# Kernel tuning notes

Hardware: AMD Instinct MI355X
Metric: run time of the kernel (lower is better)

The kernel has to match this reference:

```python
import jax, jax.numpy as jnp
import numpy as np

B, T, S = 256, 32, 128
I, H, O = 256, 1024, 256


def setup_inputs() -> dict:
    key = jax.random.key(0)
    ks = jax.random.split(key, 8)
    sc = 0.02
    return {
        "shifted_target": jax.random.normal(ks[0], (B, T, I), jnp.float32),
        "encoder_outputs": jax.random.normal(ks[1], (B, S, H), jnp.float32),
        "W_ih": jax.random.normal(ks[2], (4 * H, I), jnp.float32) * sc,
        "W_hh": jax.random.normal(ks[3], (4 * H, H), jnp.float32) * sc,
        "b_ih": jax.random.normal(ks[4], (4 * H,), jnp.float32) * sc,
        "b_hh": jax.random.normal(ks[5], (4 * H,), jnp.float32) * sc,
        "W_fc": jax.random.normal(ks[6], (O, 2 * H), jnp.float32) * sc,
        "b_fc": jax.random.normal(ks[7], (O,), jnp.float32) * sc,
    }


def reference(shifted_target, encoder_outputs, W_ih, W_hh, b_ih, b_hh, W_fc, b_fc):
    bs, tgt_len, inp = shifted_target.shape
    hid = encoder_outputs.shape[-1]
    # torch code feeds zeros (not shifted_target[:,0]) at t=0, with zero init state
    xs = shifted_target.at[:, 0, :].set(0.0)
    xs = jnp.swapaxes(xs, 0, 1)  # [T, B, I]

    def step(carry, x_t):
        h, c = carry
        gates = x_t @ W_ih.T + b_ih + h @ W_hh.T + b_hh  # [B, 4H]
        i, f, g, o = jnp.split(gates, 4, axis=-1)
        i = jax.nn.sigmoid(i)
        f = jax.nn.sigmoid(f)
        g = jnp.tanh(g)
        o = jax.nn.sigmoid(o)
        c = f * c + i * g
        h = o * jnp.tanh(c)
        # dot-product attention against encoder states
        score = jnp.einsum('bh,bsh->bs', h, encoder_outputs)
        prob = jax.nn.softmax(score, axis=-1)
        ctx = jnp.einsum('bs,bsh->bh', prob, encoder_outputs)
        out_t = jnp.concatenate([ctx, h], axis=-1) @ W_fc.T + b_fc
        return (h, c), (out_t, prob)

    h0 = jnp.zeros((bs, hid), shifted_target.dtype)
    c0 = jnp.zeros((bs, hid), shifted_target.dtype)
    _, (outs, probs) = jax.lax.scan(step, (h0, c0), xs)
    return jnp.swapaxes(outs, 0, 1), jnp.swapaxes(probs, 0, 1)
```

## Files before the change

### kernel.cpp

```cpp
#include <hip/hip_runtime.h>
#include <math.h>

#define B_  256
#define T_  32
#define S_  128
#define I_  256
#define H_  1024
#define O_  256
#define G4  4096
#define K2  2048

typedef __attribute__((ext_vector_type(8))) short bf16x8;
typedef __attribute__((ext_vector_type(4))) float f32x4;
typedef __attribute__((ext_vector_type(4))) unsigned u32x4;

#define MFMA16(a, b, c) __builtin_amdgcn_mfma_f32_16x16x32_bf16(a, b, c, 0, 0, 0)

__device__ __forceinline__ unsigned short f2bf(float f) {
    unsigned int u = __float_as_uint(f);
    u = (u + 0x7FFFu + ((u >> 16) & 1u)) >> 16;
    return (unsigned short)u;
}
__device__ __forceinline__ float sigm(float x) { return 1.0f / (1.0f + __expf(-x)); }

__device__ __forceinline__ void stg_sys128(unsigned short* p, u32x4 v) {
    asm volatile("global_store_dwordx4 %0, %1, off sc0 sc1"
                 :: "v"(p), "v"(v) : "memory");
}
__device__ __forceinline__ unsigned ldg_flag(const unsigned* p) {
    unsigned r;
    asm volatile("global_load_dword %0, %1, off sc0 sc1\n\ts_waitcnt vmcnt(0)"
                 : "=v"(r) : "v"(p) : "memory");
    return r;
}
__device__ __forceinline__ void stg_flag(unsigned* p, unsigned v) {
    asm volatile("global_store_dword %0, %1, off sc0 sc1"
                 :: "v"(p), "v"(v) : "memory");
}

__global__ void prep_kernel(
    const float* __restrict__ x, const float* __restrict__ enc,
    const float* __restrict__ Wih, const float* __restrict__ Whh,
    const float* __restrict__ bih, const float* __restrict__ bhh,
    const float* __restrict__ Wfc,
    unsigned short* __restrict__ WihR, unsigned short* __restrict__ WhhR,
    unsigned short* __restrict__ WfcR, float* __restrict__ biasR,
    unsigned short* __restrict__ xs, unsigned short* __restrict__ encB,
    unsigned short* __restrict__ h0,
    unsigned* __restrict__ bar)
{
    if (blockIdx.x == 0 && threadIdx.x < 256) bar[threadIdx.x] = 0u;

    const long NWHH = (long)G4 * H_;
    const long NWIH = (long)G4 * I_;
    const long NWFC = (long)O_ * K2;
    const long NB   = G4;
    const long NX   = (long)B_ * T_ * I_;
    const long NE   = (long)B_ * S_ * H_;
    const long NH   = (long)B_ * H_;
    const long total = NWHH + NWIH + NWFC + NB + NX + NE + NH;
    for (long i = (long)blockIdx.x * blockDim.x + threadIdx.x; i < total;
         i += (long)gridDim.x * blockDim.x) {
        long j = i;
        if (j < NE) { encB[j] = f2bf(enc[j]); continue; }
        j -= NE;
        if (j < NWHH) {
            int r = (int)(j >> 10), k = (int)(j & 1023);
            int n = ((r & 1023) << 2) | (r >> 10);
            WhhR[(long)n * H_ + k] = f2bf(Whh[j]);
            continue;
        }
        j -= NWHH;
        if (j < NWIH) {
            int r = (int)(j >> 8), k = (int)(j & 255);
            int n = ((r & 1023) << 2) | (r >> 10);
            WihR[(long)n * I_ + k] = f2bf(Wih[j]);
            continue;
        }
        j -= NWIH;
        if (j < NWFC) { WfcR[j] = f2bf(Wfc[j]); continue; }
        j -= NWFC;
        if (j < NB) {
            int r = (int)j;
            int n = ((r & 1023) << 2) | (r >> 10);
            biasR[n] = bih[r] + bhh[r];
            continue;
        }
        j -= NB;
        if (j < NX) {
            int t = (int)((j >> 8) & 31);
            xs[j] = (t == 0) ? (unsigned short)0 : f2bf(x[j]);
            continue;
        }
        j -= NX;
        h0[j] = 0;
    }
}

__global__ __launch_bounds__(512, 2) void steps_kernel(
    const unsigned short* __restrict__ xs,
    const unsigned short* __restrict__ WihR,
    const unsigned short* __restrict__ WhhR,
    const float* __restrict__ biasR,
    const unsigned short* __restrict__ h0b,
    unsigned short* __restrict__ hall,
    unsigned* __restrict__ bar)
{
    __shared__ unsigned short Wlds[64 * 1024];
    __shared__ float Gs[64 * 68];
    __shared__ unsigned short Hs[64 * 16];

    const int tid = threadIdx.x;
    const int lane = tid & 63, wave = tid >> 6;
    const int quad = lane >> 4, l16 = lane & 15;
    const int wm = wave >> 2, wn = wave & 3;

    const int id = blockIdx.x;
    const int xcd = id & 7, slot = id >> 3;
    const int nt = slot >> 2, mt = slot & 3;
    const int n0 = (xcd * 8 + nt) * 64;
    const int m0 = mt * 64;

    unsigned* myflag = bar + mt * 64 + xcd * 8 + nt;
    const unsigned* gflags = bar + mt * 64;

    for (int i = 0; i < 16; i++) {
        int q = i * 512 + tid;
        int row = q >> 7, kc = q & 127;
        int e = kc * 8;
        int de = row * 1024 + (e ^ ((row & 7) << 3));
        *(u32x4*)(Wlds + de) = *(const u32x4*)(WhhR + (long)(n0 + row) * H_ + e);
    }

    const int nw = n0 + wn * 16 + l16;
    bf16x8 bwx[8];
    {
        const unsigned short* px = WihR + (long)nw * I_ + quad * 8;
#pragma unroll
        for (int kk = 0; kk < 8; kk++) bwx[kk] = *(const bf16x8*)(px + kk * 32);
    }
    const float bj = biasR[nw];

    const unsigned short* bbase = Wlds + (wn * 16 + l16) * 1024;
    const int swz = (l16 & 7) << 3;

    int arow[2];
    const unsigned short* xrow[2];
#pragma unroll
    for (int i = 0; i < 2; i++) {
        arow[i] = m0 + wm * 32 + i * 16 + l16;
        xrow[i] = xs + (long)arow[i] * T_ * I_ + quad * 8;
    }

    float c_reg[2] = {0.f, 0.f};

    __syncthreads();

#pragma unroll 1
    for (int t = 0; t < T_; t++) {
        const f32x4 z = {0.f, 0.f, 0.f, 0.f};
        f32x4 acc[2] = {z, z};

        {
            bf16x8 a[8][2];
#pragma unroll
            for (int kk = 0; kk < 8; kk++)
#pragma unroll
                for (int i = 0; i < 2; i++)
                    a[kk][i] = *(const bf16x8*)(xrow[i] + (long)t * I_ + kk * 32);
#pragma unroll
            for (int kk = 0; kk < 8; kk++)
#pragma unroll
                for (int i = 0; i < 2; i++)
                    acc[i] = MFMA16(a[kk][i], bwx[kk], acc[i]);
        }

        if (t > 0) {
            if (tid < 64) {
                int spins = 0;
                while (ldg_flag(gflags + tid) < (unsigned)t &&
                       spins < (1 << 20)) {
                    __builtin_amdgcn_s_sleep(1);
                    ++spins;
                }
            }
            __syncthreads();
        }

        const unsigned short* hb;
        long hstr;
        if (t == 0) { hb = h0b;                      hstr = H_; }
        else        { hb = hall + (long)(t - 1) * H_; hstr = (long)T_ * H_; }
        const unsigned short* rp0 = hb + (long)arow[0] * hstr + quad * 8;
        const unsigned short* rp1 = hb + (long)arow[1] * hstr + quad * 8;

        {
            bf16x8 aa[2][4][2];
#pragma unroll
            for (int kk = 0; kk < 4; kk++) {
                aa[0][kk][0] = *(const bf16x8*)(rp0 + kk * 32);
                aa[0][kk][1] = *(const bf16x8*)(rp1 + kk * 32);
            }
#pragma unroll
            for (int sc = 0; sc < 8; sc++) {
                const int cur = sc & 1, nxt = cur ^ 1;
                if (sc < 7) {
                    const int kb = (sc + 1) * 4;
#pragma unroll
                    for (int kk = 0; kk < 4; kk++) {
                        aa[nxt][kk][0] = *(const bf16x8*)(rp0 + (kb + kk) * 32);
                        aa[nxt][kk][1] = *(const bf16x8*)(rp1 + (kb + kk) * 32);
                    }
                }
#pragma unroll
                for (int kk = 0; kk < 4; kk++) {
                    int e = ((sc * 4 + kk) * 32 + quad * 8) ^ swz;
                    bf16x8 bb = *(const bf16x8*)(bbase + e);
                    acc[0] = MFMA16(aa[cur][kk][0], bb, acc[0]);
                    acc[1] = MFMA16(aa[cur][kk][1], bb, acc[1]);
                }
            }
        }

#pragma unroll
        for (int i = 0; i < 2; i++)
#pragma unroll
            for (int r = 0; r < 4; r++)
                Gs[(wm * 32 + i * 16 + quad * 4 + r) * 68 + wn * 16 + l16] =
                    acc[i][r] + bj;
        __syncthreads();

#pragma unroll
        for (int j = 0; j < 2; j++) {
            int p = j * 512 + tid;
            int row = p >> 4, u = p & 15;
            float gi = Gs[row * 68 + u * 4 + 0];
            float gf = Gs[row * 68 + u * 4 + 1];
            float gg = Gs[row * 68 + u * 4 + 2];
            float go = Gs[row * 68 + u * 4 + 3];
            float ii = sigm(gi), ff = sigm(gf), g3 = tanhf(gg), oo = sigm(go);
            float cn = ff * c_reg[j] + ii * g3;
            float hh = oo * tanhf(cn);
            c_reg[j] = cn;
            Hs[row * 16 + u] = f2bf(hh);
        }
        __syncthreads();

        if (tid < 128) {
            int row = tid >> 1, half = tid & 1;
            u32x4 v = *(const u32x4*)(Hs + row * 16 + half * 8);
            unsigned short* dst = hall +
                ((long)(m0 + row) * T_ + t) * H_ + (n0 >> 2) + half * 8;
            stg_sys128(dst, v);
        }

        if (t < T_ - 1) {
            asm volatile("s_waitcnt vmcnt(0)" ::: "memory");
            __syncthreads();
            if (tid == 0) stg_flag(myflag, (unsigned)(t + 1));
        }
    }
}

__global__ __launch_bounds__(256) void scores_kernel(
    const unsigned short* __restrict__ hall,
    const unsigned short* __restrict__ encB,
    float* __restrict__ probs,
    unsigned short* __restrict__ PB)
{
    __shared__ float Sc[32 * 132];

    const int tid = threadIdx.x;
    const int lane = tid & 63, wave = tid >> 6;
    const int quad = lane >> 4, l16 = lane & 15;
    const int b = blockIdx.x;
    const int nw = wave;

    const unsigned short* pa0 = hall + ((long)b * T_ + l16) * H_ + quad * 8;
    const unsigned short* pa1 = hall + ((long)b * T_ + 16 + l16) * H_ + quad * 8;
    const unsigned short* pb0 = encB + ((long)b * S_ + nw * 32 + l16) * H_ + quad * 8;
    const unsigned short* pb1 = pb0 + 16 * H_;

    const f32x4 z = {0.f, 0.f, 0.f, 0.f};
    f32x4 acc00 = z, acc01 = z, acc10 = z, acc11 = z;

#pragma unroll 4
    for (int k0 = 0; k0 < H_; k0 += 32) {
        bf16x8 a0 = *(const bf16x8*)(pa0 + k0);
        bf16x8 a1 = *(const bf16x8*)(pa1 + k0);
        bf16x8 b0 = *(const bf16x8*)(pb0 + k0);
        bf16x8 b1 = *(const bf16x8*)(pb1 + k0);
        acc00 = MFMA16(a0, b0, acc00);
        acc01 = MFMA16(a0, b1, acc01);
        acc10 = MFMA16(a1, b0, acc10);
        acc11 = MFMA16(a1, b1, acc11);
    }
#pragma unroll
    for (int r = 0; r < 4; r++) {
        int row0 = quad * 4 + r;
        int col0 = nw * 32 + l16;
        Sc[row0 * 132 + col0]            = acc00[r];
        Sc[row0 * 132 + col0 + 16]       = acc01[r];
        Sc[(row0 + 16) * 132 + col0]      = acc10[r];
        Sc[(row0 + 16) * 132 + col0 + 16] = acc11[r];
    }
    __syncthreads();
    for (int r = 0; r < 8; r++) {
        int row = wave * 8 + r;
        float v0 = Sc[row * 132 + lane];
        float v1 = Sc[row * 132 + 64 + lane];
        float mx = fmaxf(v0, v1);
#pragma unroll
        for (int off = 32; off > 0; off >>= 1) mx = fmaxf(mx, __shfl_xor(mx, off));
        float e0 = __expf(v0 - mx), e1 = __expf(v1 - mx);
        float s = e0 + e1;
#pragma unroll
        for (int off = 32; off > 0; off >>= 1) s += __shfl_xor(s, off);
        float inv = 1.0f / s;
        float p0 = e0 * inv, p1 = e1 * inv;
        long o = ((long)b * T_ + row) * S_;
        probs[o + lane] = p0;
        probs[o + 64 + lane] = p1;
        PB[o + lane] = f2bf(p0);
        PB[o + 64 + lane] = f2bf(p1);
    }
}

__global__ __launch_bounds__(256) void ctx_kernel(
    const unsigned short* __restrict__ encB,
    const unsigned short* __restrict__ PB,
    unsigned short* __restrict__ ctxo)
{
    __shared__ unsigned short Es[S_ * 256];

    const int tid = threadIdx.x;
    const int lane = tid & 63, wave = tid >> 6;
    const int quad = lane >> 4, l16 = lane & 15;
    const int b = blockIdx.x;
    const int h0 = blockIdx.y * 256;

    for (int i = tid; i < S_ * 32; i += 256) {
        int s = i >> 5, hc = (i & 31) * 8;
        *(u32x4*)(Es + s * 256 + hc) =
            *(const u32x4*)(encB + ((long)b * S_ + s) * H_ + h0 + hc);
    }
    bf16x8 a[2][4];
#pragma unroll
    for (int i = 0; i < 2; i++)
#pragma unroll
        for (int ks = 0; ks < 4; ks++)
            a[i][ks] = *(const bf16x8*)(PB + ((long)b * T_ + i * 16 + l16) * S_ +
                                        ks * 32 + quad * 8);
    __syncthreads();

    f32x4 acc[2][4];
    const f32x4 z = {0.f, 0.f, 0.f, 0.f};
#pragma unroll
    for (int i = 0; i < 2; i++)
#pragma unroll
        for (int j = 0; j < 4; j++) acc[i][j] = z;

    const int cw = wave * 64;
#pragma unroll
    for (int ks = 0; ks < 4; ks++) {
        const int kb = ks * 32 + quad * 8;
#pragma unroll
        for (int j = 0; j < 4; j++) {
            const int col = cw + j * 16 + l16;
            bf16x8 bb;
#pragma unroll
            for (int e = 0; e < 8; e++) bb[e] = (short)Es[(kb + e) * 256 + col];
            acc[0][j] = MFMA16(a[0][ks], bb, acc[0][j]);
            acc[1][j] = MFMA16(a[1][ks], bb, acc[1][j]);
        }
    }
#pragma unroll
    for (int i = 0; i < 2; i++)
#pragma unroll
        for (int j = 0; j < 4; j++)
#pragma unroll
            for (int r = 0; r < 4; r++) {
                int row = i * 16 + quad * 4 + r;
                int col = h0 + cw + j * 16 + l16;
                ctxo[((long)b * T_ + row) * H_ + col] = f2bf(acc[i][j][r]);
            }
}

__global__ __launch_bounds__(256) void fc_kernel(
    const unsigned short* __restrict__ ctxo,
    const unsigned short* __restrict__ hall,
    const unsigned short* __restrict__ WfcR,
    const float* __restrict__ bfc,
    float* __restrict__ out)
{
    __shared__ __align__(16) unsigned short As[64 * 40];
    __shared__ __align__(16) unsigned short Bs[128 * 40];

    const int tid = threadIdx.x;
    const int lane = tid & 63, wave = tid >> 6;
    const int wm = wave >> 1, wn = wave & 1;
    const int quad = lane >> 4, l16 = lane & 15;
    const int n0 = blockIdx.x * 128, m0 = blockIdx.y * 64;

    const int arow = tid >> 2, akc = (tid & 3) * 8;
    const int brow = tid >> 1, bkc = (tid & 1) * 16;

    f32x4 acc[2][4];
    const f32x4 z = {0.f, 0.f, 0.f, 0.f};
#pragma unroll
    for (int i = 0; i < 2; i++)
#pragma unroll
        for (int j = 0; j < 4; j++) acc[i][j] = z;

    for (int k0 = 0; k0 < K2; k0 += 32) {
        const unsigned short* asrc = (k0 < H_)
            ? ctxo + (long)(m0 + arow) * H_ + k0 + akc
            : hall + (long)(m0 + arow) * H_ + (k0 - H_) + akc;
        *(u32x4*)(As + arow * 40 + akc) = *(const u32x4*)asrc;
        const unsigned short* src = WfcR + (long)(n0 + brow) * K2 + k0 + bkc;
        *(u32x4*)(Bs + brow * 40 + bkc)     = *(const u32x4*)src;
        *(u32x4*)(Bs + brow * 40 + bkc + 8) = *(const u32x4*)(src + 8);
        __syncthreads();
        bf16x8 a0 = *(const bf16x8*)(As + (wm * 32 + l16) * 40 + quad * 8);
        bf16x8 a1 = *(const bf16x8*)(As + (wm * 32 + 16 + l16) * 40 + quad * 8);
#pragma unroll
        for (int j = 0; j < 4; j++) {
            bf16x8 bb = *(const bf16x8*)(Bs + (wn * 64 + j * 16 + l16) * 40 + quad * 8);
            acc[0][j] = MFMA16(a0, bb, acc[0][j]);
            acc[1][j] = MFMA16(a1, bb, acc[1][j]);
        }
        __syncthreads();
    }
#pragma unroll
    for (int i = 0; i < 2; i++)
#pragma unroll
        for (int j = 0; j < 4; j++)
#pragma unroll
            for (int r = 0; r < 4; r++) {
                int row = m0 + wm * 32 + i * 16 + quad * 4 + r;
                int col = n0 + wn * 64 + j * 16 + l16;
                out[(long)row * O_ + col] = acc[i][j][r] + bfc[col];
            }
}

extern "C" void kernel_launch(void* const* d_in, const int* in_sizes, int n_in,
                              void* d_out, int out_size, void* d_ws, size_t ws_size,
                              hipStream_t stream) {
    const float* x   = (const float*)d_in[0];
    const float* enc = (const float*)d_in[1];
    const float* Wih = (const float*)d_in[2];
    const float* Whh = (const float*)d_in[3];
    const float* bih = (const float*)d_in[4];
    const float* bhh = (const float*)d_in[5];
    const float* Wfc = (const float*)d_in[6];
    const float* bfc = (const float*)d_in[7];
    float* out = (float*)d_out;

    char* ws = (char*)d_ws;
    unsigned short* WIHR = (unsigned short*)(ws + 0);
    unsigned short* WHHR = (unsigned short*)(ws + 2097152);
    unsigned short* WFCR = (unsigned short*)(ws + 10485760);
    float*          BIAS = (float*)         (ws + 11534336);
    unsigned short* XS   = (unsigned short*)(ws + 11550720);
    unsigned short* H0   = (unsigned short*)(ws + 15745024);
    unsigned*       BAR  = (unsigned*)      (ws + 16793600);
    unsigned short* HALL = (unsigned short*)(ws + 17842176);
    unsigned short* ENCB = (unsigned short*)(ws + 34619392);
    unsigned short* PB   = (unsigned short*)(ws + 101728256);
    unsigned short* CTX  = (unsigned short*)(ws + 103825408);

    prep_kernel<<<8192, 256, 0, stream>>>(x, enc, Wih, Whh, bih, bhh, Wfc,
                                          WIHR, WHHR, WFCR, BIAS, XS, ENCB,
                                          H0, BAR);

    {
        void* args[] = {(void*)&XS, (void*)&WIHR, (void*)&WHHR, (void*)&BIAS,
                        (void*)&H0, (void*)&HALL, (void*)&BAR};
        (void)hipLaunchCooperativeKernel(reinterpret_cast<void*>(steps_kernel),
                                         dim3(256), dim3(512), args, 0, stream);
    }

    scores_kernel<<<B_, 256, 0, stream>>>(HALL, ENCB,
                                          out + (long)B_ * T_ * O_, PB);
    ctx_kernel<<<dim3(B_, 4), 256, 0, stream>>>(ENCB, PB, CTX);
    fc_kernel<<<dim3(2, 128), 256, 0, stream>>>(CTX, HALL, WFCR, bfc, out);
}
```

Before: 998.5 us.

## Vectorize prep conversion, skip h0 matmul at t=0, fuse scores and ctx kernels

The prep kernel now converts four floats per thread with float4 loads and ushort4 stores instead of one element per thread, and its grid is halved. The recurrent kernel skips the h·W_hh product at t=0, since the initial hidden state is zero. The scores and ctx kernels are merged into one attention kernel that keeps the bf16 probabilities in shared memory, which removes the PB round trip through global memory and one launch. The price is that each block of the fused kernel now walks all four H chunks serially with 256 blocks instead of 1024, and it uses more shared memory, which lowers occupancy.

```diff
diff --git a/kernel.cpp b/kernel.cpp
--- a/kernel.cpp
+++ b/kernel.cpp
@@ -51,49 +51,76 @@
 {
     if (blockIdx.x == 0 && threadIdx.x < 256) bar[threadIdx.x] = 0u;
 
-    const long NWHH = (long)G4 * H_;
-    const long NWIH = (long)G4 * I_;
-    const long NWFC = (long)O_ * K2;
-    const long NB   = G4;
-    const long NX   = (long)B_ * T_ * I_;
-    const long NE   = (long)B_ * S_ * H_;
-    const long NH   = (long)B_ * H_;
-    const long total = NWHH + NWIH + NWFC + NB + NX + NE + NH;
+    const long NE4   = (long)B_ * S_ * H_ / 4;
+    const long NWHH4 = (long)G4 * H_ / 4;
+    const long NWIH4 = (long)G4 * I_ / 4;
+    const long NWFC4 = (long)O_ * K2 / 4;
+    const long NX4   = (long)B_ * T_ * I_ / 4;
+    const long NH4   = (long)B_ * H_ / 4;
+    const long NB    = G4;
+    const long total = NE4 + NWHH4 + NWIH4 + NWFC4 + NX4 + NH4 + NB;
     for (long i = (long)blockIdx.x * blockDim.x + threadIdx.x; i < total;
          i += (long)gridDim.x * blockDim.x) {
         long j = i;
-        if (j < NE) { encB[j] = f2bf(enc[j]); continue; }
-        j -= NE;
-        if (j < NWHH) {
-            int r = (int)(j >> 10), k = (int)(j & 1023);
+        if (j < NE4) {
+            float4 v = *(const float4*)(enc + j * 4);
+            ushort4 o = {f2bf(v.x), f2bf(v.y), f2bf(v.z), f2bf(v.w)};
+            *(ushort4*)(encB + j * 4) = o;
+            continue;
+        }
+        j -= NE4;
+        if (j < NWHH4) {
+            long e = j * 4;
+            int r = (int)(e >> 10), k = (int)(e & 1023);
             int n = ((r & 1023) << 2) | (r >> 10);
-            WhhR[(long)n * H_ + k] = f2bf(Whh[j]);
+            float4 v = *(const float4*)(Whh + e);
+            ushort4 o = {f2bf(v.x), f2bf(v.y), f2bf(v.z), f2bf(v.w)};
+            *(ushort4*)(WhhR + (long)n * H_ + k) = o;
             continue;
         }
-        j -= NWHH;
-        if (j < NWIH) {
-            int r = (int)(j >> 8), k = (int)(j & 255);
+        j -= NWHH4;
+        if (j < NWIH4) {
+            long e = j * 4;
+            int r = (int)(e >> 8), k = (int)(e & 255);
             int n = ((r & 1023) << 2) | (r >> 10);
-            WihR[(long)n * I_ + k] = f2bf(Wih[j]);
+            float4 v = *(const float4*)(Wih + e);
+            ushort4 o = {f2bf(v.x), f2bf(v.y), f2bf(v.z), f2bf(v.w)};
+            *(ushort4*)(WihR + (long)n * I_ + k) = o;
             continue;
         }
-        j -= NWIH;
-        if (j < NWFC) { WfcR[j] = f2bf(Wfc[j]); continue; }
-        j -= NWFC;
-        if (j < NB) {
+        j -= NWIH4;
+        if (j < NWFC4) {
+            long e = j * 4;
+            float4 v = *(const float4*)(Wfc + e);
+            ushort4 o = {f2bf(v.x), f2bf(v.y), f2bf(v.z), f2bf(v.w)};
+            *(ushort4*)(WfcR + e) = o;
+            continue;
+        }
+        j -= NWFC4;
+        if (j < NX4) {
+            long e = j * 4;
+            int t = (int)((e >> 8) & 31);
+            ushort4 o = {0, 0, 0, 0};
+            if (t != 0) {
+                float4 v = *(const float4*)(x + e);
+                o.x = f2bf(v.x); o.y = f2bf(v.y);
+                o.z = f2bf(v.z); o.w = f2bf(v.w);
+            }
+            *(ushort4*)(xs + e) = o;
+            continue;
+        }
+        j -= NX4;
+        if (j < NH4) {
+            ushort4 zz = {0, 0, 0, 0};
+            *(ushort4*)(h0 + j * 4) = zz;
+            continue;
+        }
+        j -= NH4;
+        {
             int r = (int)j;
             int n = ((r & 1023) << 2) | (r >> 10);
             biasR[n] = bih[r] + bhh[r];
-            continue;
-        }
-        j -= NB;
-        if (j < NX) {
-            int t = (int)((j >> 8) & 31);
-            xs[j] = (t == 0) ? (unsigned short)0 : f2bf(x[j]);
-            continue;
-        }
-        j -= NX;
-        h0[j] = 0;
+        }
     }
 }
 
@@ -185,16 +212,12 @@
                 }
             }
             __syncthreads();
-        }
-
-        const unsigned short* hb;
-        long hstr;
-        if (t == 0) { hb = h0b;                      hstr = H_; }
-        else        { hb = hall + (long)(t - 1) * H_; hstr = (long)T_ * H_; }
-        const unsigned short* rp0 = hb + (long)arow[0] * hstr + quad * 8;
-        const unsigned short* rp1 = hb + (long)arow[1] * hstr + quad * 8;
-
-        {
+
+            const unsigned short* hb = hall + (long)(t - 1) * H_;
+            const long hstr = (long)T_ * H_;
+            const unsigned short* rp0 = hb + (long)arow[0] * hstr + quad * 8;
+            const unsigned short* rp1 = hb + (long)arow[1] * hstr + quad * 8;
+
             bf16x8 aa[2][4][2];
 #pragma unroll
             for (int kk = 0; kk < 4; kk++) {
@@ -262,13 +285,15 @@
     }
 }
 
-__global__ __launch_bounds__(256) void scores_kernel(
+__global__ __launch_bounds__(256) void attn_kernel(
     const unsigned short* __restrict__ hall,
     const unsigned short* __restrict__ encB,
     float* __restrict__ probs,
-    unsigned short* __restrict__ PB)
+    unsigned short* __restrict__ ctxo)
 {
     __shared__ float Sc[32 * 132];
+    __shared__ unsigned short Ps[32 * 128];
+    __shared__ unsigned short Es[S_ * 256];
 
     const int tid = threadIdx.x;
     const int lane = tid & 63, wave = tid >> 6;
@@ -321,69 +346,59 @@
         long o = ((long)b * T_ + row) * S_;
         probs[o + lane] = p0;
         probs[o + 64 + lane] = p1;
-        PB[o + lane] = f2bf(p0);
-        PB[o + 64 + lane] = f2bf(p1);
-    }
-}
-
-__global__ __launch_bounds__(256) void ctx_kernel(
-    const unsigned short* __restrict__ encB,
-    const unsigned short* __restrict__ PB,
-    unsigned short* __restrict__ ctxo)
-{
-    __shared__ unsigned short Es[S_ * 256];
-
-    const int tid = threadIdx.x;
-    const int lane = tid & 63, wave = tid >> 6;
-    const int quad = lane >> 4, l16 = lane & 15;
-    const int b = blockIdx.x;
-    const int h0 = blockIdx.y * 256;
-
-    for (int i = tid; i < S_ * 32; i += 256) {
-        int s = i >> 5, hc = (i & 31) * 8;
-        *(u32x4*)(Es + s * 256 + hc) =
-            *(const u32x4*)(encB + ((long)b * S_ + s) * H_ + h0 + hc);
-    }
+        Ps[row * 128 + lane] = f2bf(p0);
+        Ps[row * 128 + 64 + lane] = f2bf(p1);
+    }
+    __syncthreads();
+
     bf16x8 a[2][4];
 #pragma unroll
     for (int i = 0; i < 2; i++)
 #pragma unroll
         for (int ks = 0; ks < 4; ks++)
-            a[i][ks] = *(const bf16x8*)(PB + ((long)b * T_ + i * 16 + l16) * S_ +
+            a[i][ks] = *(const bf16x8*)(Ps + (i * 16 + l16) * 128 +
                                         ks * 32 + quad * 8);
-    __syncthreads();
-
-    f32x4 acc[2][4];
-    const f32x4 z = {0.f, 0.f, 0.f, 0.f};
-#pragma unroll
-    for (int i = 0; i < 2; i++)
-#pragma unroll
-        for (int j = 0; j < 4; j++) acc[i][j] = z;
 
     const int cw = wave * 64;
-#pragma unroll
-    for (int ks = 0; ks < 4; ks++) {
-        const int kb = ks * 32 + quad * 8;
-#pragma unroll
-        for (int j = 0; j < 4; j++) {
-            const int col = cw + j * 16 + l16;
-            bf16x8 bb;
-#pragma unroll
-            for (int e = 0; e < 8; e++) bb[e] = (short)Es[(kb + e) * 256 + col];
-            acc[0][j] = MFMA16(a[0][ks], bb, acc[0][j]);
-            acc[1][j] = MFMA16(a[1][ks], bb, acc[1][j]);
-        }
-    }
-#pragma unroll
-    for (int i = 0; i < 2; i++)
-#pragma unroll
-        for (int j = 0; j < 4; j++)
-#pragma unroll
-            for (int r = 0; r < 4; r++) {
-                int row = i * 16 + quad * 4 + r;
-                int col = h0 + cw + j * 16 + l16;
-                ctxo[((long)b * T_ + row) * H_ + col] = f2bf(acc[i][j][r]);
+    for (int hc = 0; hc < 4; hc++) {
+        if (hc) __syncthreads();
+        for (int i = tid; i < S_ * 32; i += 256) {
+            int s = i >> 5, hcc = (i & 31) * 8;
+            *(u32x4*)(Es + s * 256 + hcc) =
+                *(const u32x4*)(encB + ((long)b * S_ + s) * H_ + hc * 256 + hcc);
+        }
+        __syncthreads();
+
+        f32x4 acc[2][4];
+#pragma unroll
+        for (int i = 0; i < 2; i++)
+#pragma unroll
+            for (int j = 0; j < 4; j++) acc[i][j] = z;
+
+#pragma unroll
+        for (int ks = 0; ks < 4; ks++) {
+            const int kb = ks * 32 + quad * 8;
+#pragma unroll
+            for (int j = 0; j < 4; j++) {
+                const int col = cw + j * 16 + l16;
+                bf16x8 bb;
+#pragma unroll
+                for (int e = 0; e < 8; e++) bb[e] = (short)Es[(kb + e) * 256 + col];
+                acc[0][j] = MFMA16(a[0][ks], bb, acc[0][j]);
+                acc[1][j] = MFMA16(a[1][ks], bb, acc[1][j]);
             }
+        }
+#pragma unroll
+        for (int i = 0; i < 2; i++)
+#pragma unroll
+            for (int j = 0; j < 4; j++)
+#pragma unroll
+                for (int r = 0; r < 4; r++) {
+                    int row = i * 16 + quad * 4 + r;
+                    int col = hc * 256 + cw + j * 16 + l16;
+                    ctxo[((long)b * T_ + row) * H_ + col] = f2bf(acc[i][j][r]);
+                }
+    }
 }
 
 __global__ __launch_bounds__(256) void fc_kernel(
@@ -466,10 +481,9 @@
     unsigned*       BAR  = (unsigned*)      (ws + 16793600);
     unsigned short* HALL = (unsigned short*)(ws + 17842176);
     unsigned short* ENCB = (unsigned short*)(ws + 34619392);
-    unsigned short* PB   = (unsigned short*)(ws + 101728256);
     unsigned short* CTX  = (unsigned short*)(ws + 103825408);
 
-    prep_kernel<<<8192, 256, 0, stream>>>(x, enc, Wih, Whh, bih, bhh, Wfc,
+    prep_kernel<<<4096, 256, 0, stream>>>(x, enc, Wih, Whh, bih, bhh, Wfc,
                                           WIHR, WHHR, WFCR, BIAS, XS, ENCB,
                                           H0, BAR);
 
@@ -480,8 +494,7 @@
                                          dim3(256), dim3(512), args, 0, stream);
     }
 
-    scores_kernel<<<B_, 256, 0, stream>>>(HALL, ENCB,
-                                          out + (long)B_ * T_ * O_, PB);
-    ctx_kernel<<<dim3(B_, 4), 256, 0, stream>>>(ENCB, PB, CTX);
+    attn_kernel<<<B_, 256, 0, stream>>>(HALL, ENCB,
+                                        out + (long)B_ * T_ * O_, CTX);
     fc_kernel<<<dim3(2, 128), 256, 0, stream>>>(CTX, HALL, WFCR, bfc, out);
 }
```

New measurement: 967.8 us. -3.1%, faster.
